# Optimization experiments

Measured on AMD Instinct MI355X. Metric: run time of the kernel, lower is better.

Reference implementation:

```python
import jax, jax.numpy as jnp
import numpy as np

BIN_SIZE = 128
DIST_MULT = 0.1
LN_EPS = 1e-6


def setup_inputs() -> dict:
    key = jax.random.key(0)
    ks = jax.random.split(key, 24)
    B, N, D, DD, H = 8, 25600, 256, 128, 128
    s = 0.02
    inp = {
        'x': jax.random.normal(ks[0], (B, N, D), dtype=jnp.float32),
        'msk': jax.random.randint(ks[1], (B, N), 0, 2) > 0,
        'ln_g': jnp.ones((D,), jnp.float32),
        'ln_b': jnp.zeros((D,), jnp.float32),
        # ffn_dist: Linear(256,128) ELU Linear(128,128) ELU Linear(128,128)
        'w1': s * jax.random.normal(ks[2], (D, H), jnp.float32),
        'b1': jnp.zeros((H,), jnp.float32),
        'w2': s * jax.random.normal(ks[3], (H, H), jnp.float32),
        'b2': jnp.zeros((H,), jnp.float32),
        'w3': s * jax.random.normal(ks[4], (H, DD), jnp.float32),
        'b3': jnp.zeros((DD,), jnp.float32),
        # LSH codebook random rotations [distance_dim, max_num_bins//2]
        'codebook': jax.random.normal(ks[5], (DD, 100), jnp.float32),
        # two GHConvDense layers, hidden_dim=output_dim=256
        'theta0': jax.random.normal(ks[6], (D, D), jnp.float32) * s,
        'wh0': jax.random.normal(ks[7], (D, D), jnp.float32) * s,
        'wt0': jax.random.normal(ks[8], (D, D), jnp.float32) * s,
        'bt0': jnp.zeros((D,), jnp.float32),
        'theta1': jax.random.normal(ks[9], (D, D), jnp.float32) * s,
        'wh1': jax.random.normal(ks[10], (D, D), jnp.float32) * s,
        'wt1': jax.random.normal(ks[11], (D, D), jnp.float32) * s,
        'bt1': jnp.zeros((D,), jnp.float32),
    }
    return inp


def _forward(x, msk, ln_g, ln_b, w1, b1, w2, b2, w3, b3, codebook,
             theta0, wh0, wt0, bt0, theta1, wh1, wt1, bt1):
    B, n_elems, D = x.shape
    pad = (-n_elems) % BIN_SIZE  # static python int
    if pad:
        x = jnp.pad(x, ((0, 0), (0, pad), (0, 0)))
        msk = jnp.pad(msk, ((0, 0), (0, pad)), constant_values=True)
    Np = n_elems + pad
    n_bins = Np // BIN_SIZE

    # layernorm
    mu = jnp.mean(x, -1, keepdims=True)
    var = jnp.mean(jnp.square(x - mu), -1, keepdims=True)
    xn = (x - mu) * jax.lax.rsqrt(var + LN_EPS) * ln_g + ln_b

    # distance FFN + dist activation (elu)
    h = jax.nn.elu(xn @ w1 + b1)
    h = jax.nn.elu(h @ w2 + b2)
    x_dist = jax.nn.elu(h @ w3 + b3)  # [B, Np, distance_dim]

    # LSH binning
    mul = x_dist @ codebook[:, :max(1, n_bins // 2)]
    cmul = jnp.concatenate([mul, -mul], axis=-1)  # [B, Np, n_bins]
    a = jnp.argmax(cmul, axis=-1)
    bin_idx = a + jnp.where(msk, 0, n_bins - 1)
    bins_split = jnp.argsort(bin_idx, axis=-1)  # [B, Np]

    # gather into bins
    xm = jnp.take_along_axis(x_dist, bins_split[..., None], axis=1)
    xm = xm.reshape(B, n_bins, BIN_SIZE, x_dist.shape[-1])
    xb = jnp.take_along_axis(xn, bins_split[..., None], axis=1)
    xb = xb.reshape(B, n_bins, BIN_SIZE, D)
    mskf = jnp.take_along_axis(msk, bins_split, axis=1)
    mskf = mskf.reshape(B, n_bins, BIN_SIZE, 1).astype(x.dtype)

    # pairwise Gaussian kernel within each bin
    xk = xm * mskf
    nsq = jnp.sum(jnp.square(xk), -1)  # [B, nb, P]
    inner = jnp.einsum('bnpd,bnqd->bnpq', xk, xk)
    d2 = nsq[..., :, None] - 2.0 * inner + nsq[..., None, :]
    dist = jnp.sqrt(jnp.clip(d2, 1e-6, 1e6))
    dm = jnp.clip(jnp.exp(-DIST_MULT * dist), 0.0, 1.0)
    dm = dm * mskf * jnp.swapaxes(mskf, -1, -2)  # mask rows & cols [B,nb,P,P]

    # gated graph convolutions
    for th, wh, wt, bt in ((theta0, wh0, wt0, bt0), (theta1, wh1, wt1, bt1)):
        xmk = xb * mskf
        f_hom = jnp.einsum('bnpq,bnqd->bnpd', dm, (xmk @ th) * mskf)
        f_het = xmk @ wh
        gate = jax.nn.sigmoid(xb @ wt + bt)
        xb = jax.nn.elu(gate * f_hom + (1.0 - gate) * f_het) * mskf

    # reverse LSH scatter
    xb_flat = xb.reshape(B, Np, D)
    ret = jax.vmap(lambda idx, pts: jnp.zeros((Np, D), pts.dtype).at[idx].set(pts))(
        bins_split, xb_flat)
    return ret[:, :n_elems, :]


def reference(x, msk, ln_g, ln_b, w1, b1, w2, b2, w3, b3, codebook,
              theta0, wh0, wt0, bt0, theta1, wh1, wt1, bt1):
    return _forward(x, msk, ln_g, ln_b, w1, b1, w2, b2, w3, b3, codebook,
                    theta0, wh0, wt0, bt0, theta1, wh1, wt1, bt1)
```

## Files before the change

kernel.cpp:

```cpp
#include <hip/hip_runtime.h>
#include <math.h>

#define B_ 8
#define NP_ 25600
#define T_ (B_*NP_)
#define D_ 256
#define H_ 128
#define DD_ 128
#define NBINS_ 200
#define NIDS_ 400
#define PB_ 128
#define NC_ 100
#define GT_ (B_*NBINS_)

typedef __attribute__((ext_vector_type(8))) short bf16x8;
typedef __attribute__((ext_vector_type(4))) float f32x4;
typedef __attribute__((ext_vector_type(4))) unsigned short u16x4;
typedef unsigned short u16;

__device__ __forceinline__ float eluf(float v){ return v > 0.f ? v : expm1f(v); }
__device__ __forceinline__ u16 f2bf(float f){
  union { float f; unsigned u; } v; v.f = f;
  unsigned r = v.u + 0x7fffu + ((v.u >> 16) & 1u);
  return (u16)(r >> 16);
}
__device__ __forceinline__ float bf2f(u16 h){
  union { unsigned u; float f; } v; v.u = ((unsigned)h) << 16; return v.f;
}

__device__ __forceinline__ void gl16(void* lds, const void* g){
  __builtin_amdgcn_global_load_lds((const __attribute__((address_space(1))) void*)g,
                                   (__attribute__((address_space(3))) void*)lds, 16, 0, 0);
}

__global__ void k_mask_detect(const unsigned int* __restrict__ m, int* __restrict__ flags){
  int any_f1 = 0, any_o = 0;
  for (int i = blockIdx.x*blockDim.x + threadIdx.x; i < T_/4; i += gridDim.x*blockDim.x){
    unsigned int w = m[i];
    if (w == 0x3F800000u) any_f1 = 1;
    else if (w > 1u) any_o = 1;
  }
  if (any_f1) atomicOr(&flags[0], 1);
  if (any_o)  atomicOr(&flags[1], 1);
}

__global__ void k_mask_convert(const void* __restrict__ m, const int* __restrict__ flags,
                               float* __restrict__ mskf){
  int i = blockIdx.x*256 + threadIdx.x;
  int mode = flags[0] ? 2 : (flags[1] ? 1 : 0);
  bool v;
  if (mode == 2)      v = ((const float*)m)[i] != 0.f;
  else if (mode == 1) v = ((const unsigned char*)m)[i] != 0;
  else                v = ((const int*)m)[i] != 0;
  mskf[i] = v ? 1.f : 0.f;
}

__global__ __launch_bounds__(256) void k_ln(const float* __restrict__ x,
    const float* __restrict__ g, const float* __restrict__ b, float* __restrict__ xn){
  const int wave = threadIdx.x >> 6, lane = threadIdx.x & 63;
  const long t = (long)blockIdx.x*4 + wave;
  float4 v = ((const float4*)(x + t*D_))[lane];
  float s  = v.x + v.y + v.z + v.w;
  float s2 = v.x*v.x + v.y*v.y + v.z*v.z + v.w*v.w;
  #pragma unroll
  for (int o = 32; o; o >>= 1){ s += __shfl_xor(s, o); s2 += __shfl_xor(s2, o); }
  const float mu = s * (1.f/D_);
  float var = s2*(1.f/D_) - mu*mu;
  var = fmaxf(var, 0.f);
  const float rs = rsqrtf(var + 1e-6f);
  float4 gg = ((const float4*)g)[lane];
  float4 bb = ((const float4*)b)[lane];
  float4 o4;
  o4.x = (v.x-mu)*rs*gg.x + bb.x;
  o4.y = (v.y-mu)*rs*gg.y + bb.y;
  o4.z = (v.z-mu)*rs*gg.z + bb.z;
  o4.w = (v.w-mu)*rs*gg.w + bb.w;
  ((float4*)(xn + t*D_))[lane] = o4;
}

template<int K>
__global__ __launch_bounds__(256) void k_gemm2(const float* __restrict__ A,
    const float* __restrict__ W, const float* __restrict__ bias, float* __restrict__ C){
  __shared__ __align__(16) float As[32*132];
  __shared__ __align__(16) float Bs[32*132];
  const size_t m0 = (size_t)blockIdx.x * 128;
  const int tid = threadIdx.x;
  const int tm = tid >> 4, tn = tid & 15;
  float acc[8][8] = {};
  for (int kc = 0; kc < K; kc += 32){
    __syncthreads();
    {
      const int r = tid >> 1, kq = (tid & 1) * 16;
      const float* src = &A[(m0 + r)*(size_t)K + kc + kq];
      #pragma unroll
      for (int q = 0; q < 4; ++q){
        const float4 v = ((const float4*)src)[q];
        As[(kq + q*4 + 0)*132 + r] = v.x;
        As[(kq + q*4 + 1)*132 + r] = v.y;
        As[(kq + q*4 + 2)*132 + r] = v.z;
        As[(kq + q*4 + 3)*132 + r] = v.w;
      }
      const int kk = tid >> 3, n0 = (tid & 7) * 16;
      const float* wsrc = &W[(size_t)(kc + kk)*128 + n0];
      #pragma unroll
      for (int q = 0; q < 4; ++q)
        *(float4*)&Bs[kk*132 + n0 + q*4] = ((const float4*)wsrc)[q];
    }
    __syncthreads();
    #pragma unroll
    for (int k = 0; k < 32; ++k){
      float a[8], b[8];
      *(float4*)&a[0] = *(const float4*)&As[k*132 + tm*8];
      *(float4*)&a[4] = *(const float4*)&As[k*132 + tm*8 + 4];
      *(float4*)&b[0] = *(const float4*)&Bs[k*132 + tn*8];
      *(float4*)&b[4] = *(const float4*)&Bs[k*132 + tn*8 + 4];
      #pragma unroll
      for (int i = 0; i < 8; ++i)
        #pragma unroll
        for (int j = 0; j < 8; ++j)
          acc[i][j] = fmaf(a[i], b[j], acc[i][j]);
    }
  }
  #pragma unroll
  for (int i = 0; i < 8; ++i){
    const size_t row = m0 + tm*8 + i;
    #pragma unroll
    for (int q = 0; q < 2; ++q){
      float4 o;
      o.x = eluf(acc[i][q*4+0] + bias[tn*8 + q*4+0]);
      o.y = eluf(acc[i][q*4+1] + bias[tn*8 + q*4+1]);
      o.z = eluf(acc[i][q*4+2] + bias[tn*8 + q*4+2]);
      o.w = eluf(acc[i][q*4+3] + bias[tn*8 + q*4+3]);
      *(float4*)&C[row*128 + tn*8 + q*4] = o;
    }
  }
}

__global__ void k_cbpad(const float* __restrict__ cb, float* __restrict__ cbp){
  const int k = blockIdx.x, c = threadIdx.x;
  cbp[k*128 + c] = (c < NC_) ? cb[k*NC_ + c] : 0.f;
}

__global__ __launch_bounds__(256) void k_mulmax(const float* __restrict__ A,
    const float* __restrict__ CB, const float* __restrict__ mskf, int* __restrict__ bidx){
  __shared__ __align__(16) float As[32*132];
  __shared__ __align__(16) float Bs[32*132];
  const size_t m0 = (size_t)blockIdx.x * 128;
  const int tid = threadIdx.x;
  const int tm = tid >> 4, tn = tid & 15;
  float acc[8][8] = {};
  for (int kc = 0; kc < DD_; kc += 32){
    __syncthreads();
    {
      const int r = tid >> 1, kq = (tid & 1) * 16;
      const float* src = &A[(m0 + r)*(size_t)DD_ + kc + kq];
      #pragma unroll
      for (int q = 0; q < 4; ++q){
        const float4 v = ((const float4*)src)[q];
        As[(kq + q*4 + 0)*132 + r] = v.x;
        As[(kq + q*4 + 1)*132 + r] = v.y;
        As[(kq + q*4 + 2)*132 + r] = v.z;
        As[(kq + q*4 + 3)*132 + r] = v.w;
      }
      const int kk = tid >> 3, n0 = (tid & 7) * 16;
      const float* wsrc = &CB[(size_t)(kc + kk)*128 + n0];
      #pragma unroll
      for (int q = 0; q < 4; ++q)
        *(float4*)&Bs[kk*132 + n0 + q*4] = ((const float4*)wsrc)[q];
    }
    __syncthreads();
    #pragma unroll
    for (int k = 0; k < 32; ++k){
      float a[8], b[8];
      *(float4*)&a[0] = *(const float4*)&As[k*132 + tm*8];
      *(float4*)&a[4] = *(const float4*)&As[k*132 + tm*8 + 4];
      *(float4*)&b[0] = *(const float4*)&Bs[k*132 + tn*8];
      *(float4*)&b[4] = *(const float4*)&Bs[k*132 + tn*8 + 4];
      #pragma unroll
      for (int i = 0; i < 8; ++i)
        #pragma unroll
        for (int j = 0; j < 8; ++j)
          acc[i][j] = fmaf(a[i], b[j], acc[i][j]);
    }
  }
  #pragma unroll
  for (int i = 0; i < 8; ++i){
    float bv = -1e30f; int bi = 0;
    #pragma unroll
    for (int j = 0; j < 8; ++j){
      const int c = tn*8 + j;
      if (c < NC_){
        const float v = acc[i][j];
        if (v > bv || (v == bv && c < bi)){ bv = v; bi = c; }
        const float nv = -v; const int nc2 = c + NC_;
        if (nv > bv || (nv == bv && nc2 < bi)){ bv = nv; bi = nc2; }
      }
    }
    #pragma unroll
    for (int o = 1; o < 16; o <<= 1){
      const float ov = __shfl_xor(bv, o);
      const int oi = __shfl_xor(bi, o);
      if (ov > bv || (ov == bv && oi < bi)){ bv = ov; bi = oi; }
    }
    if (tn == 0){
      const size_t t = m0 + tm*8 + i;
      bidx[t] = bi + (mskf[t] != 0.f ? 0 : NBINS_ - 1);
    }
  }
}

__global__ void k_hist(const int* __restrict__ bidx, int* __restrict__ hist){
  const int i = blockIdx.x*256 + threadIdx.x;
  const int b = i / NP_;
  atomicAdd(&hist[b*NIDS_ + bidx[i]], 1);
}

__global__ void k_prefix(const int* __restrict__ hist, int* __restrict__ offs){
  const int b = threadIdx.x;
  if (b < B_){
    int run = 0;
    for (int v = 0; v < NIDS_; ++v){ offs[b*NIDS_ + v] = run; run += hist[b*NIDS_ + v]; }
  }
}

__global__ __launch_bounds__(64) void k_binsort(const int* __restrict__ bidx,
    const int* __restrict__ offs, const int* __restrict__ hist, int* __restrict__ split){
  const int bv = blockIdx.x;
  if (hist[bv] == 0) return;
  const int b = bv / NIDS_, v = bv % NIDS_;
  int base = offs[bv];
  const int lane = threadIdx.x;
  const int* row = bidx + b*NP_;
  for (int i0 = 0; i0 < NP_; i0 += 64){
    const int i = i0 + lane;
    const bool m = (row[i] == v);
    const unsigned long long mk = __ballot(m);
    if (m){
      const int pos = base + __popcll(mk & ((1ull << lane) - 1ull));
      split[b*NP_ + pos] = i;
    }
    base += __popcll(mk);
  }
}

__global__ __launch_bounds__(256) void k_gather(const float* __restrict__ xn,
    const float* __restrict__ xd, const float* __restrict__ mskf,
    const int* __restrict__ split, u16* __restrict__ xmh,
    u16* __restrict__ xkh, float* __restrict__ mskg){
  const long j = (long)blockIdx.x*4 + (threadIdx.x >> 6);
  const int lane = threadIdx.x & 63;
  const int b = (int)(j / NP_);
  const int i = split[j];
  const long src = (long)b*NP_ + i;
  const float mv = mskf[src];
  const float4 v = ((const float4*)(xn + src*D_))[lane];
  u16x4 o;
  o[0] = f2bf(v.x*mv); o[1] = f2bf(v.y*mv); o[2] = f2bf(v.z*mv); o[3] = f2bf(v.w*mv);
  ((u16x4*)(xmh + j*D_))[lane] = o;
  if (lane < 32){
    const float4 ww = ((const float4*)(xd + src*DD_))[lane];
    u16x4 ow;
    ow[0] = f2bf(ww.x*mv); ow[1] = f2bf(ww.y*mv); ow[2] = f2bf(ww.z*mv); ow[3] = f2bf(ww.w*mv);
    ((u16x4*)(xkh + j*DD_))[lane] = ow;
  }
  if (lane == 0) mskg[j] = mv;
}

__global__ __launch_bounds__(256) void k_wt(const float* __restrict__ W, u16* __restrict__ o){
  const int n = blockIdx.x, k = threadIdx.x;
  o[n*D_ + k] = f2bf(W[k*D_ + n]);
}
__global__ __launch_bounds__(256) void k_wt2(const float* __restrict__ wt,
    const float* __restrict__ wh, u16* __restrict__ o){
  const int n = blockIdx.x, k = threadIdx.x;
  const float v = (n < 256) ? wt[(size_t)k*D_ + n] : wh[(size_t)k*D_ + (n-256)];
  o[(size_t)n*D_ + k] = f2bf(v);
}

__device__ __forceinline__ void stage64a(const u16* __restrict__ g, size_t row0,
    int ld, int k0, u16* Ls, int tid){
  const int w = tid >> 6, l = tid & 63;
  #pragma unroll
  for (int s = 0; s < 4; ++s){
    const int G = (s*4 + w)*64 + l;
    const int r = G >> 3, c8 = G & 7;
    gl16(&Ls[G*8], &g[(row0 + r)*(size_t)ld + k0 + ((c8 ^ (r & 7))*8)]);
  }
}
__device__ __forceinline__ void stage128a(const u16* __restrict__ g, size_t row0,
    int ld, u16* Ls, int tid){
  const int w = tid >> 6, l = tid & 63;
  #pragma unroll
  for (int s = 0; s < 8; ++s){
    const int G = (s*4 + w)*64 + l;
    const int r = G >> 4, c8 = G & 15;
    gl16(&Ls[G*8], &g[(row0 + r)*(size_t)ld + ((c8 ^ (r & 7))*8)]);
  }
}
__device__ __forceinline__ bf16x8 ldf(const u16* Ls, int row, int c8, int ldc8){
  return *(const bf16x8*)&Ls[(row*ldc8 + (c8 ^ (row & 7)))*8];
}

__global__ __launch_bounds__(256) void k_dm(const u16* __restrict__ xk,
    const float* __restrict__ rm, u16* __restrict__ dmb){
  __shared__ __align__(16) u16 Xs[128*128];
  __shared__ float nsq[128];
  __shared__ float msl[128];
  const int g = blockIdx.x;
  const int tid = threadIdx.x, l = tid & 63, wid = tid >> 6;
  const int wr = wid >> 1, wc = wid & 1, lm = l & 15, lk = l >> 4;
  stage128a(xk, (size_t)g*128, DD_, Xs, tid);
  if (tid < 128) msl[tid] = rm[(size_t)g*128 + tid];
  __syncthreads();
  f32x4 acc[4][4] = {};
  #pragma unroll
  for (int ks = 0; ks < 4; ++ks){
    bf16x8 a[4], b[4];
    #pragma unroll
    for (int mi = 0; mi < 4; ++mi) a[mi] = ldf(Xs, wr*64 + mi*16 + lm, ks*4 + lk, 16);
    #pragma unroll
    for (int ni = 0; ni < 4; ++ni) b[ni] = ldf(Xs, wc*64 + ni*16 + lm, ks*4 + lk, 16);
    #pragma unroll
    for (int mi = 0; mi < 4; ++mi)
      #pragma unroll
      for (int ni = 0; ni < 4; ++ni)
        acc[mi][ni] = __builtin_amdgcn_mfma_f32_16x16x32_bf16(a[mi], b[ni], acc[mi][ni], 0, 0, 0);
  }
  if (wr == wc && ((lm >> 2) == lk)){
    #pragma unroll
    for (int mi = 0; mi < 4; ++mi)
      nsq[wr*64 + mi*16 + lm] = acc[mi][mi][lm & 3];
  }
  __syncthreads();
  #pragma unroll
  for (int mi = 0; mi < 4; ++mi)
    #pragma unroll
    for (int ni = 0; ni < 4; ++ni)
      #pragma unroll
      for (int r = 0; r < 4; ++r){
        const int row = wr*64 + mi*16 + lk*4 + r;
        const int col = wc*64 + ni*16 + lm;
        float d2 = nsq[row] + nsq[col] - 2.f*acc[mi][ni][r];
        d2 = fminf(fmaxf(d2, 1e-6f), 1e6f);
        float w = expf(-0.1f * sqrtf(d2));
        w = fminf(w, 1.f);
        dmb[((size_t)g*PB_ + row)*PB_ + col] = f2bf(w * msl[row] * msl[col]);
      }
}

__global__ __launch_bounds__(256) void k_gg(const u16* __restrict__ X,
    const u16* __restrict__ WT, u16* __restrict__ o){
  __shared__ __align__(16) u16 As[128*64];
  __shared__ __align__(16) u16 Bs[128*64];
  const int n0 = blockIdx.x * 128;
  const size_t r0 = (size_t)blockIdx.y * 128;
  const int tid = threadIdx.x, l = tid & 63, wid = tid >> 6;
  const int wr = wid >> 1, wc = wid & 1, lm = l & 15, lk = l >> 4;
  f32x4 acc[4][4] = {};
  for (int kt = 0; kt < 4; ++kt){
    if (kt) __syncthreads();
    stage64a(X,  r0,          D_, kt*64, As, tid);
    stage64a(WT, (size_t)n0,  D_, kt*64, Bs, tid);
    __syncthreads();
    #pragma unroll
    for (int ks = 0; ks < 2; ++ks){
      bf16x8 a[4], b[4];
      #pragma unroll
      for (int mi = 0; mi < 4; ++mi) a[mi] = ldf(As, wr*64 + mi*16 + lm, ks*4 + lk, 8);
      #pragma unroll
      for (int ni = 0; ni < 4; ++ni) b[ni] = ldf(Bs, wc*64 + ni*16 + lm, ks*4 + lk, 8);
      #pragma unroll
      for (int mi = 0; mi < 4; ++mi)
        #pragma unroll
        for (int ni = 0; ni < 4; ++ni)
          acc[mi][ni] = __builtin_amdgcn_mfma_f32_16x16x32_bf16(a[mi], b[ni], acc[mi][ni], 0, 0, 0);
    }
  }
  #pragma unroll
  for (int mi = 0; mi < 4; ++mi)
    #pragma unroll
    for (int ni = 0; ni < 4; ++ni)
      #pragma unroll
      for (int r = 0; r < 4; ++r){
        const int row = wr*64 + mi*16 + lk*4 + r;
        const int col = wc*64 + ni*16 + lm;
        o[(r0 + row)*512 + n0 + col] = f2bf(acc[mi][ni][r]);
      }
}

template<int OUT>
__global__ __launch_bounds__(256) void k_tbmix(const u16* __restrict__ dmb,
    const u16* __restrict__ thT, const u16* __restrict__ X,
    const u16* __restrict__ atah, const float* __restrict__ btv,
    const int* __restrict__ split, u16* __restrict__ o16, float* __restrict__ o32){
  __shared__ __align__(16) u16 bufA[128*128];
  __shared__ __align__(16) u16 bufB[128*128];
  __shared__ int ssp[128];
  const int h = blockIdx.x, g = blockIdx.y;
  const int tid = threadIdx.x, l = tid & 63, wid = tid >> 6;
  const int wr = wid >> 1, wc = wid & 1, lm = l & 15, lk = l >> 4;
  u16* SA = bufA;
  u16* SB = bufA + 128*64;
  if (OUT){ if (tid < 128) ssp[tid] = split[g*128 + tid]; }
  f32x4 acc1[4][4] = {};
  for (int kt = 0; kt < 4; ++kt){
    if (kt) __syncthreads();
    stage64a(thT, (size_t)h*128, D_, kt*64, SA, tid);
    stage64a(X,   (size_t)g*128, D_, kt*64, SB, tid);
    __syncthreads();
    #pragma unroll
    for (int ks = 0; ks < 2; ++ks){
      bf16x8 a[4], b[4];
      #pragma unroll
      for (int mi = 0; mi < 4; ++mi) a[mi] = ldf(SA, wr*64 + mi*16 + lm, ks*4 + lk, 8);
      #pragma unroll
      for (int ni = 0; ni < 4; ++ni) b[ni] = ldf(SB, wc*64 + ni*16 + lm, ks*4 + lk, 8);
      #pragma unroll
      for (int mi = 0; mi < 4; ++mi)
        #pragma unroll
        for (int ni = 0; ni < 4; ++ni)
          acc1[mi][ni] = __builtin_amdgcn_mfma_f32_16x16x32_bf16(a[mi], b[ni], acc1[mi][ni], 0, 0, 0);
    }
  }
  __syncthreads();
  #pragma unroll
  for (int mi = 0; mi < 4; ++mi)
    #pragma unroll
    for (int ni = 0; ni < 4; ++ni)
      #pragma unroll
      for (int r = 0; r < 4; ++r){
        const int row = wr*64 + mi*16 + lk*4 + r;
        const int col = wc*64 + ni*16 + lm;
        bufB[(row*16 + ((col >> 3) ^ (row & 7)))*8 + (col & 7)] = f2bf(acc1[mi][ni][r]);
      }
  stage128a(dmb, (size_t)g*128, PB_, bufA, tid);
  __syncthreads();
  f32x4 acc[4][4] = {};
  #pragma unroll
  for (int ks = 0; ks < 4; ++ks){
    bf16x8 a[4], b[4];
    #pragma unroll
    for (int mi = 0; mi < 4; ++mi) a[mi] = ldf(bufA, wr*64 + mi*16 + lm, ks*4 + lk, 16);
    #pragma unroll
    for (int ni = 0; ni < 4; ++ni) b[ni] = ldf(bufB, wc*64 + ni*16 + lm, ks*4 + lk, 16);
    #pragma unroll
    for (int mi = 0; mi < 4; ++mi)
      #pragma unroll
      for (int ni = 0; ni < 4; ++ni)
        acc[mi][ni] = __builtin_amdgcn_mfma_f32_16x16x32_bf16(a[mi], b[ni], acc[mi][ni], 0, 0, 0);
  }
  __syncthreads();
  {
    const int w = tid >> 6, ll = tid & 63;
    #pragma unroll
    for (int s = 0; s < 8; ++s){
      const int G = (s*4 + w)*64 + ll;
      const int r = G >> 4, c8 = G & 15;
      const size_t gbase = ((size_t)g*128 + r)*512 + h*128 + c8*8;
      gl16(&bufA[G*8], &atah[gbase]);
      gl16(&bufB[G*8], &atah[gbase + 256]);
    }
  }
  __syncthreads();
  #pragma unroll
  for (int mi = 0; mi < 4; ++mi)
    #pragma unroll
    for (int ni = 0; ni < 4; ++ni){
      const int colc = wc*64 + ni*16 + lm;
      const int gc = h*128 + colc;
      const float bb = btv[gc];
      #pragma unroll
      for (int r = 0; r < 4; ++r){
        const int row = wr*64 + mi*16 + lk*4 + r;
        const float at = bf2f(bufA[row*128 + colc]);
        const float ahv = bf2f(bufB[row*128 + colc]);
        const float gt = 1.f/(1.f + expf(-(at + bb)));
        const float o = eluf(gt*acc[mi][ni][r] + (1.f - gt)*ahv);
        if (OUT == 0){
          o16[((size_t)g*128 + row)*D_ + gc] = f2bf(o);
        } else {
          const int b = g / NBINS_;
          o32[((size_t)b*NP_ + ssp[row])*D_ + gc] = o;
        }
      }
    }
}

extern "C" void kernel_launch(void* const* d_in, const int* in_sizes, int n_in,
                              void* d_out, int out_size, void* d_ws, size_t ws_size,
                              hipStream_t stream){
  (void)in_sizes; (void)n_in; (void)out_size;
  const float* x    = (const float*)d_in[0];
  const void*  msk  = d_in[1];
  const float* ln_g = (const float*)d_in[2];
  const float* ln_b = (const float*)d_in[3];
  const float* w1 = (const float*)d_in[4];
  const float* b1 = (const float*)d_in[5];
  const float* w2 = (const float*)d_in[6];
  const float* b2 = (const float*)d_in[7];
  const float* w3 = (const float*)d_in[8];
  const float* b3 = (const float*)d_in[9];
  const float* cb = (const float*)d_in[10];
  const float* th0 = (const float*)d_in[11];
  const float* wh0 = (const float*)d_in[12];
  const float* wt0 = (const float*)d_in[13];
  const float* bt0 = (const float*)d_in[14];
  const float* th1 = (const float*)d_in[15];
  const float* wh1 = (const float*)d_in[16];
  const float* wt1 = (const float*)d_in[17];
  const float* bt1 = (const float*)d_in[18];
  float* out = (float*)d_out;

  char* ws = (char*)d_ws;
  size_t off = 0;
  auto alloc = [&](size_t bytes) -> void* {
    void* p = ws + off; off += (bytes + 255) & ~(size_t)255; return p;
  };
  int* flags = (int*)alloc(2*sizeof(int));
  int* hist  = (int*)alloc((size_t)B_*NIDS_*4);
  int* offs  = (int*)alloc((size_t)B_*NIDS_*4);
  int* bidx  = (int*)alloc((size_t)T_*4);
  int* split = (int*)alloc((size_t)T_*4);
  float* mskf = (float*)alloc((size_t)T_*4);
  float* mskg = (float*)alloc((size_t)T_*4);
  float* cbp = (float*)alloc((size_t)128*128*4);
  u16* thT0 = (u16*)alloc((size_t)D_*D_*2);
  u16* thT1 = (u16*)alloc((size_t)D_*D_*2);
  u16* wtwh0 = (u16*)alloc((size_t)512*D_*2);
  u16* wtwh1 = (u16*)alloc((size_t)512*D_*2);
  char* regA = (char*)alloc((size_t)T_*512*2);
  u16* xmh = (u16*)alloc((size_t)T_*D_*2);
  char* regC = (char*)alloc((size_t)T_*D_*2);
  u16* xb1 = (u16*)alloc((size_t)T_*D_*2);
  if (off > ws_size) return;

  float* P = (float*)regA;
  float* Q = P + (size_t)T_*DD_;
  u16* atah = (u16*)regA;
  u16* xkh = (u16*)regC;
  u16* dmb = xkh + (size_t)T_*DD_;
  float* xn = out;

  hipMemsetAsync(flags, 0, 2*sizeof(int), stream);
  hipMemsetAsync(hist, 0, (size_t)B_*NIDS_*4, stream);

  k_mask_detect<<<64, 256, 0, stream>>>((const unsigned int*)msk, flags);
  k_mask_convert<<<T_/256, 256, 0, stream>>>(msk, flags, mskf);

  k_ln<<<T_/4, 256, 0, stream>>>(x, ln_g, ln_b, xn);

  k_cbpad<<<128, 128, 0, stream>>>(cb, cbp);
  k_wt<<<256, 256, 0, stream>>>(th0, thT0);
  k_wt<<<256, 256, 0, stream>>>(th1, thT1);
  k_wt2<<<512, 256, 0, stream>>>(wt0, wh0, wtwh0);
  k_wt2<<<512, 256, 0, stream>>>(wt1, wh1, wtwh1);

  k_gemm2<D_><<<T_/128, 256, 0, stream>>>(xn, w1, b1, P);
  k_gemm2<H_><<<T_/128, 256, 0, stream>>>(P, w2, b2, Q);
  k_gemm2<H_><<<T_/128, 256, 0, stream>>>(Q, w3, b3, P);

  k_mulmax<<<T_/128, 256, 0, stream>>>(P, cbp, mskf, bidx);
  k_hist<<<T_/256, 256, 0, stream>>>(bidx, hist);
  k_prefix<<<1, 64, 0, stream>>>(hist, offs);
  k_binsort<<<B_*NIDS_, 64, 0, stream>>>(bidx, offs, hist, split);

  k_gather<<<T_/4, 256, 0, stream>>>(xn, P, mskf, split, xmh, xkh, mskg);
  k_dm<<<GT_, 256, 0, stream>>>(xkh, mskg, dmb);

  k_gg<<<dim3(4, T_/128), 256, 0, stream>>>(xmh, wtwh0, atah);
  k_tbmix<0><<<dim3(2, GT_), 256, 0, stream>>>(dmb, thT0, xmh, atah, bt0, nullptr, xb1, nullptr);

  k_gg<<<dim3(4, T_/128), 256, 0, stream>>>(xb1, wtwh1, atah);
  k_tbmix<1><<<dim3(2, GT_), 256, 0, stream>>>(dmb, thT1, xb1, atah, bt1, split, nullptr, out);
}
```

Baseline: 1.440 ms.

## Fuse gate/heterophily GEMM into graph-mix kernel and interleave FP32 GEMM thread tiles

Removes the separate k_gg kernel that wrote the gate and heterophily projections (atah) to global memory. k_fuse now computes X@wt and X@wh in registers per block and keeps them as packed bf16 for the epilogue, which avoids a large bf16 intermediate write and read per layer. The cost is more register pressure from two extra accumulator sets, with launch_bounds set to 256,2, and a third staging loop. Separately, the FP32 SIMT GEMMs now give each thread two interleaved 4-wide row and column strips instead of one contiguous 8-wide strip, to reduce LDS bank conflicts.

```diff
diff --git a/kernel.cpp b/kernel.cpp
--- a/kernel.cpp
+++ b/kernel.cpp
@@ -110,10 +110,10 @@
     #pragma unroll
     for (int k = 0; k < 32; ++k){
       float a[8], b[8];
-      *(float4*)&a[0] = *(const float4*)&As[k*132 + tm*8];
-      *(float4*)&a[4] = *(const float4*)&As[k*132 + tm*8 + 4];
-      *(float4*)&b[0] = *(const float4*)&Bs[k*132 + tn*8];
-      *(float4*)&b[4] = *(const float4*)&Bs[k*132 + tn*8 + 4];
+      *(float4*)&a[0] = *(const float4*)&As[k*132 + tm*4];
+      *(float4*)&a[4] = *(const float4*)&As[k*132 + 64 + tm*4];
+      *(float4*)&b[0] = *(const float4*)&Bs[k*132 + tn*4];
+      *(float4*)&b[4] = *(const float4*)&Bs[k*132 + 64 + tn*4];
       #pragma unroll
       for (int i = 0; i < 8; ++i)
         #pragma unroll
@@ -123,15 +123,16 @@
   }
   #pragma unroll
   for (int i = 0; i < 8; ++i){
-    const size_t row = m0 + tm*8 + i;
+    const size_t row = m0 + (i < 4 ? tm*4 + i : 64 + tm*4 + (i-4));
     #pragma unroll
     for (int q = 0; q < 2; ++q){
+      const int c0 = q ? 64 + tn*4 : tn*4;
       float4 o;
-      o.x = eluf(acc[i][q*4+0] + bias[tn*8 + q*4+0]);
-      o.y = eluf(acc[i][q*4+1] + bias[tn*8 + q*4+1]);
-      o.z = eluf(acc[i][q*4+2] + bias[tn*8 + q*4+2]);
-      o.w = eluf(acc[i][q*4+3] + bias[tn*8 + q*4+3]);
-      *(float4*)&C[row*128 + tn*8 + q*4] = o;
+      o.x = eluf(acc[i][q*4+0] + bias[c0+0]);
+      o.y = eluf(acc[i][q*4+1] + bias[c0+1]);
+      o.z = eluf(acc[i][q*4+2] + bias[c0+2]);
+      o.w = eluf(acc[i][q*4+3] + bias[c0+3]);
+      *(float4*)&C[row*128 + c0] = o;
     }
   }
 }
@@ -172,10 +173,10 @@
     #pragma unroll
     for (int k = 0; k < 32; ++k){
       float a[8], b[8];
-      *(float4*)&a[0] = *(const float4*)&As[k*132 + tm*8];
-      *(float4*)&a[4] = *(const float4*)&As[k*132 + tm*8 + 4];
-      *(float4*)&b[0] = *(const float4*)&Bs[k*132 + tn*8];
-      *(float4*)&b[4] = *(const float4*)&Bs[k*132 + tn*8 + 4];
+      *(float4*)&a[0] = *(const float4*)&As[k*132 + tm*4];
+      *(float4*)&a[4] = *(const float4*)&As[k*132 + 64 + tm*4];
+      *(float4*)&b[0] = *(const float4*)&Bs[k*132 + tn*4];
+      *(float4*)&b[4] = *(const float4*)&Bs[k*132 + 64 + tn*4];
       #pragma unroll
       for (int i = 0; i < 8; ++i)
         #pragma unroll
@@ -188,7 +189,7 @@
     float bv = -1e30f; int bi = 0;
     #pragma unroll
     for (int j = 0; j < 8; ++j){
-      const int c = tn*8 + j;
+      const int c = (j < 4 ? tn*4 + j : 64 + tn*4 + (j-4));
       if (c < NC_){
         const float v = acc[i][j];
         if (v > bv || (v == bv && c < bi)){ bv = v; bi = c; }
@@ -203,7 +204,7 @@
       if (ov > bv || (ov == bv && oi < bi)){ bv = ov; bi = oi; }
     }
     if (tn == 0){
-      const size_t t = m0 + tm*8 + i;
+      const size_t t = m0 + (i < 4 ? tm*4 + i : 64 + tm*4 + (i-4));
       bidx[t] = bi + (mskf[t] != 0.f ? 0 : NBINS_ - 1);
     }
   }
@@ -348,50 +349,10 @@
       }
 }
 
-__global__ __launch_bounds__(256) void k_gg(const u16* __restrict__ X,
-    const u16* __restrict__ WT, u16* __restrict__ o){
-  __shared__ __align__(16) u16 As[128*64];
-  __shared__ __align__(16) u16 Bs[128*64];
-  const int n0 = blockIdx.x * 128;
-  const size_t r0 = (size_t)blockIdx.y * 128;
-  const int tid = threadIdx.x, l = tid & 63, wid = tid >> 6;
-  const int wr = wid >> 1, wc = wid & 1, lm = l & 15, lk = l >> 4;
-  f32x4 acc[4][4] = {};
-  for (int kt = 0; kt < 4; ++kt){
-    if (kt) __syncthreads();
-    stage64a(X,  r0,          D_, kt*64, As, tid);
-    stage64a(WT, (size_t)n0,  D_, kt*64, Bs, tid);
-    __syncthreads();
-    #pragma unroll
-    for (int ks = 0; ks < 2; ++ks){
-      bf16x8 a[4], b[4];
-      #pragma unroll
-      for (int mi = 0; mi < 4; ++mi) a[mi] = ldf(As, wr*64 + mi*16 + lm, ks*4 + lk, 8);
-      #pragma unroll
-      for (int ni = 0; ni < 4; ++ni) b[ni] = ldf(Bs, wc*64 + ni*16 + lm, ks*4 + lk, 8);
-      #pragma unroll
-      for (int mi = 0; mi < 4; ++mi)
-        #pragma unroll
-        for (int ni = 0; ni < 4; ++ni)
-          acc[mi][ni] = __builtin_amdgcn_mfma_f32_16x16x32_bf16(a[mi], b[ni], acc[mi][ni], 0, 0, 0);
-    }
-  }
-  #pragma unroll
-  for (int mi = 0; mi < 4; ++mi)
-    #pragma unroll
-    for (int ni = 0; ni < 4; ++ni)
-      #pragma unroll
-      for (int r = 0; r < 4; ++r){
-        const int row = wr*64 + mi*16 + lk*4 + r;
-        const int col = wc*64 + ni*16 + lm;
-        o[(r0 + row)*512 + n0 + col] = f2bf(acc[mi][ni][r]);
-      }
-}
-
 template<int OUT>
-__global__ __launch_bounds__(256) void k_tbmix(const u16* __restrict__ dmb,
-    const u16* __restrict__ thT, const u16* __restrict__ X,
-    const u16* __restrict__ atah, const float* __restrict__ btv,
+__global__ __launch_bounds__(256, 2) void k_fuse(const u16* __restrict__ dmb,
+    const u16* __restrict__ thT, const u16* __restrict__ wtwh,
+    const u16* __restrict__ X, const float* __restrict__ btv,
     const int* __restrict__ split, u16* __restrict__ o16, float* __restrict__ o32){
   __shared__ __align__(16) u16 bufA[128*128];
   __shared__ __align__(16) u16 bufB[128*128];
@@ -399,27 +360,63 @@
   const int h = blockIdx.x, g = blockIdx.y;
   const int tid = threadIdx.x, l = tid & 63, wid = tid >> 6;
   const int wr = wid >> 1, wc = wid & 1, lm = l & 15, lk = l >> 4;
-  u16* SA = bufA;
-  u16* SB = bufA + 128*64;
+  u16* SBw = bufB;
+  u16* SBh = bufB + 128*64;
   if (OUT){ if (tid < 128) ssp[tid] = split[g*128 + tid]; }
-  f32x4 acc1[4][4] = {};
+  f32x4 at[4][4] = {}, ah[4][4] = {};
   for (int kt = 0; kt < 4; ++kt){
-    if (kt) __syncthreads();
-    stage64a(thT, (size_t)h*128, D_, kt*64, SA, tid);
-    stage64a(X,   (size_t)g*128, D_, kt*64, SB, tid);
+    __syncthreads();
+    stage64a(X,    (size_t)g*128,       D_, kt*64, bufA, tid);
+    stage64a(wtwh, (size_t)h*128,       D_, kt*64, SBw, tid);
+    stage64a(wtwh, (size_t)(256+h*128), D_, kt*64, SBh, tid);
+    __syncthreads();
+    #pragma unroll
+    for (int ks = 0; ks < 2; ++ks){
+      bf16x8 xa[4], bt_[4], bh_[4];
+      #pragma unroll
+      for (int mi = 0; mi < 4; ++mi) xa[mi] = ldf(bufA, wr*64 + mi*16 + lm, ks*4 + lk, 8);
+      #pragma unroll
+      for (int ni = 0; ni < 4; ++ni){
+        bt_[ni] = ldf(SBw, wc*64 + ni*16 + lm, ks*4 + lk, 8);
+        bh_[ni] = ldf(SBh, wc*64 + ni*16 + lm, ks*4 + lk, 8);
+      }
+      #pragma unroll
+      for (int mi = 0; mi < 4; ++mi)
+        #pragma unroll
+        for (int ni = 0; ni < 4; ++ni){
+          at[mi][ni] = __builtin_amdgcn_mfma_f32_16x16x32_bf16(xa[mi], bt_[ni], at[mi][ni], 0, 0, 0);
+          ah[mi][ni] = __builtin_amdgcn_mfma_f32_16x16x32_bf16(xa[mi], bh_[ni], ah[mi][ni], 0, 0, 0);
+        }
+    }
+  }
+  u16x4 atp[4][4], ahp[4][4];
+  #pragma unroll
+  for (int mi = 0; mi < 4; ++mi)
+    #pragma unroll
+    for (int ni = 0; ni < 4; ++ni)
+      #pragma unroll
+      for (int r = 0; r < 4; ++r){
+        atp[mi][ni][r] = f2bf(at[mi][ni][r]);
+        ahp[mi][ni][r] = f2bf(ah[mi][ni][r]);
+      }
+  f32x4 a1[4][4] = {};
+  for (int kt = 0; kt < 4; ++kt){
+    __syncthreads();
+    stage64a(thT, (size_t)h*128, D_, kt*64, bufA, tid);
+    stage64a(X,   (size_t)g*128, D_, kt*64, bufB, tid);
     __syncthreads();
     #pragma unroll
     for (int ks = 0; ks < 2; ++ks){
       bf16x8 a[4], b[4];
       #pragma unroll
-      for (int mi = 0; mi < 4; ++mi) a[mi] = ldf(SA, wr*64 + mi*16 + lm, ks*4 + lk, 8);
-      #pragma unroll
-      for (int ni = 0; ni < 4; ++ni) b[ni] = ldf(SB, wc*64 + ni*16 + lm, ks*4 + lk, 8);
+      for (int mi = 0; mi < 4; ++mi) a[mi] = ldf(bufA, wr*64 + mi*16 + lm, ks*4 + lk, 8);
+      #pragma unroll
+      for (int ni = 0; ni < 4; ++ni) b[ni] = ldf(bufB, wc*64 + ni*16 + lm, ks*4 + lk, 8);
       #pragma unroll
       for (int mi = 0; mi < 4; ++mi)
         #pragma unroll
         for (int ni = 0; ni < 4; ++ni)
-          acc1[mi][ni] = __builtin_amdgcn_mfma_f32_16x16x32_bf16(a[mi], b[ni], acc1[mi][ni], 0, 0, 0);
+          a1[mi][ni] = __builtin_amdgcn_mfma_f32_16x16x32_bf16(a[mi], b[ni], a1[mi][ni], 0, 0, 0);
     }
   }
   __syncthreads();
@@ -431,7 +428,7 @@
       for (int r = 0; r < 4; ++r){
         const int row = wr*64 + mi*16 + lk*4 + r;
         const int col = wc*64 + ni*16 + lm;
-        bufB[(row*16 + ((col >> 3) ^ (row & 7)))*8 + (col & 7)] = f2bf(acc1[mi][ni][r]);
+        bufB[(row*16 + ((col >> 3) ^ (row & 7)))*8 + (col & 7)] = f2bf(a1[mi][ni][r]);
       }
   stage128a(dmb, (size_t)g*128, PB_, bufA, tid);
   __syncthreads();
@@ -449,19 +446,6 @@
       for (int ni = 0; ni < 4; ++ni)
         acc[mi][ni] = __builtin_amdgcn_mfma_f32_16x16x32_bf16(a[mi], b[ni], acc[mi][ni], 0, 0, 0);
   }
-  __syncthreads();
-  {
-    const int w = tid >> 6, ll = tid & 63;
-    #pragma unroll
-    for (int s = 0; s < 8; ++s){
-      const int G = (s*4 + w)*64 + ll;
-      const int r = G >> 4, c8 = G & 15;
-      const size_t gbase = ((size_t)g*128 + r)*512 + h*128 + c8*8;
-      gl16(&bufA[G*8], &atah[gbase]);
-      gl16(&bufB[G*8], &atah[gbase + 256]);
-    }
-  }
-  __syncthreads();
   #pragma unroll
   for (int mi = 0; mi < 4; ++mi)
     #pragma unroll
@@ -472,9 +456,9 @@
       #pragma unroll
       for (int r = 0; r < 4; ++r){
         const int row = wr*64 + mi*16 + lk*4 + r;
-        const float at = bf2f(bufA[row*128 + colc]);
-        const float ahv = bf2f(bufB[row*128 + colc]);
-        const float gt = 1.f/(1.f + expf(-(at + bb)));
+        const float atv = bf2f(atp[mi][ni][r]);
+        const float ahv = bf2f(ahp[mi][ni][r]);
+        const float gt = 1.f/(1.f + expf(-(atv + bb)));
         const float o = eluf(gt*acc[mi][ni][r] + (1.f - gt)*ahv);
         if (OUT == 0){
           o16[((size_t)g*128 + row)*D_ + gc] = f2bf(o);
@@ -536,7 +520,6 @@
 
   float* P = (float*)regA;
   float* Q = P + (size_t)T_*DD_;
-  u16* atah = (u16*)regA;
   u16* xkh = (u16*)regC;
   u16* dmb = xkh + (size_t)T_*DD_;
   float* xn = out;
@@ -567,9 +550,6 @@
   k_gather<<<T_/4, 256, 0, stream>>>(xn, P, mskf, split, xmh, xkh, mskg);
   k_dm<<<GT_, 256, 0, stream>>>(xkh, mskg, dmb);
 
-  k_gg<<<dim3(4, T_/128), 256, 0, stream>>>(xmh, wtwh0, atah);
-  k_tbmix<0><<<dim3(2, GT_), 256, 0, stream>>>(dmb, thT0, xmh, atah, bt0, nullptr, xb1, nullptr);
-
-  k_gg<<<dim3(4, T_/128), 256, 0, stream>>>(xb1, wtwh1, atah);
-  k_tbmix<1><<<dim3(2, GT_), 256, 0, stream>>>(dmb, thT1, xb1, atah, bt1, split, nullptr, out);
-}
+  k_fuse<0><<<dim3(2, GT_), 256, 0, stream>>>(dmb, thT0, wtwh0, xmh, bt0, nullptr, xb1, nullptr);
+  k_fuse<1><<<dim3(2, GT_), 256, 0, stream>>>(dmb, thT1, wtwh1, xb1, bt1, split, nullptr, out);
+}
```

Result: faster. 1.295 ms (-10.1%).
